# Performance work log

Measured on AMD Instinct MI355X. Metric: run time of the kernel, lower is better.

Reference implementation:

```python
import jax, jax.numpy as jnp
import numpy as np

B, S, H, V, NSPK = 8, 128, 768, 30000, 8


def gru_cell(x, h, wih, whh, bih, bhh):
    # torch GRU gate order: r, z, n
    gi = x @ wih.T + bih
    gh = h @ whh.T + bhh
    i_r, i_z, i_n = jnp.split(gi, 3, axis=-1)
    h_r, h_z, h_n = jnp.split(gh, 3, axis=-1)
    r = jax.nn.sigmoid(i_r + h_r)
    z = jax.nn.sigmoid(i_z + h_z)
    n = jnp.tanh(i_n + r * h_n)
    return (1.0 - z) * n + z * h


def setup_inputs() -> dict:
    key = jax.random.key(0)
    ks = jax.random.split(key, 32)
    nrm = lambda k, shp: (jax.random.normal(k, shp, dtype=jnp.float32) * 0.02)
    inp = {
        "chat_ids": jnp.arange(B, dtype=jnp.int32),
        "speaker_info": jax.random.randint(ks[0], (B, S), 0, NSPK),
        "sp_dialogues": jax.random.randint(ks[1], (B,), 0, NSPK),
        "sp_ind": jax.random.randint(ks[2], (B,), 0, NSPK),
        "inputs": jax.random.randint(ks[3], (B, S), 0, V),
        "emb": nrm(ks[4], (V, H)),
        # rnnD: GRU(E=H -> H)
        "d_wih": nrm(ks[5], (3 * H, H)), "d_whh": nrm(ks[6], (3 * H, H)),
        "d_bih": nrm(ks[7], (3 * H,)), "d_bhh": nrm(ks[8], (3 * H,)),
        # rnnG: GRU(3E -> H)
        "g_wih": nrm(ks[9], (3 * H, 3 * H)), "g_whh": nrm(ks[10], (3 * H, H)),
        "g_bih": nrm(ks[11], (3 * H,)), "g_bhh": nrm(ks[12], (3 * H,)),
        # rnnS: GRU(2E -> 2E)
        "s_wih": nrm(ks[13], (6 * H, 2 * H)), "s_whh": nrm(ks[14], (6 * H, 2 * H)),
        "s_bih": nrm(ks[15], (6 * H,)), "s_bhh": nrm(ks[16], (6 * H,)),
        # attention projections (qembed = kembed = hidden = E)
        "wq": nrm(ks[17], (H, H)), "bq": nrm(ks[18], (H,)),
        "wk": nrm(ks[19], (H, H)), "bk": nrm(ks[20], (H,)),
        "wv": nrm(ks[21], (H, H)), "bv": nrm(ks[22], (H,)),
        # fixed random initial states (torch.randn in forward)
        "h0": jax.random.normal(ks[23], (2 * H,), dtype=jnp.float32),
        "d_h0": jax.random.normal(ks[24], (H,), dtype=jnp.float32),
        "attn_h": jax.random.normal(ks[25], (H,), dtype=jnp.float32),
    }
    return inp


def _forward(chat_ids, speaker_info, inputs, emb,
             d_wih, d_whh, d_bih, d_bhh,
             g_wih, g_whh, g_bih, g_bhh,
             s_wih, s_whh, s_bih, s_bhh,
             wq, bq, wk, bk, wv, bv, h0, d_h0, attn_h):
    bert = emb[inputs]                              # [B,S,E]

    # rnnD over the whole dialogue (dropout is identity in eval)
    def d_step(h, x):
        h2 = gru_cell(x, h, d_wih, d_whh, d_bih, d_bhh)
        return h2, h2
    _, dlg = jax.lax.scan(d_step, jnp.zeros((B, H), bert.dtype), jnp.swapaxes(bert, 0, 1))
    dialogue = jnp.swapaxes(dlg, 0, 1)              # [B,S,H]

    speaker_seq = speaker_info[chat_ids]            # [B,S]
    scale = jnp.asarray(np.sqrt(H), dtype=dialogue.dtype)
    steps = jnp.arange(S)

    def batch_step(d_h, b_in):
        dlg_b, spk_b = b_in                         # [S,H], [S]
        op_buf0 = jnp.zeros((S, H), dialogue.dtype)
        sp0 = jnp.tile(h0[None, :], (NSPK, 1))      # every speaker starts at h0

        def step(carry, xs):
            op_buf, sp_states, dh = carry
            utt, spk, s = xs
            # growing-context attention over previously written op rows
            # (row s is still zero at this point, matching fop[b][:s+1])
            q = utt @ wq.T + bq                      # [H]
            K = op_buf @ wk.T + bk                   # [S,H]
            Vv = op_buf @ wv.T + bv                  # [S,H]
            scores = (K @ q) / scale                 # [S]
            mask = steps <= s
            probs = jax.nn.softmax(jnp.where(mask, scores, -jnp.inf))
            probs = jnp.where(jnp.isnan(probs), 0.0, probs)
            attn_out = probs @ Vv                    # [H]
            attn_part = jnp.where(s == 0, attn_h, attn_out)
            tmp = jnp.concatenate([attn_part, utt])  # [2H]
            h_spk = sp_states[spk]                   # dynamic speaker state
            h_new = gru_cell(tmp, h_spk, s_wih, s_whh, s_bih, s_bhh)
            spop_s = h_new + tmp                     # spop[b][s] = out + tmp
            sp_states = sp_states.at[spk].set(h_new)
            fop2_s = jnp.concatenate([spop_s, utt])  # [3H]
            op_s = gru_cell(fop2_s, dh, g_wih, g_whh, g_bih, g_bhh)
            op_buf = op_buf.at[s].set(op_s)
            return (op_buf, sp_states, op_s), (op_s, spop_s)

        (_, _, dh_out), (op_b, spop_b) = jax.lax.scan(
            step, (op_buf0, sp0, d_h), (dlg_b, spk_b, steps))
        return dh_out, (op_b, spop_b)

    # d_h carries across batch items, exactly as in the torch loop
    _, (op, spop) = jax.lax.scan(batch_step, d_h0, (dialogue, speaker_seq))
    return op, spop                                  # [B,S,H], [B,S,2H]


def reference(chat_ids, speaker_info, sp_dialogues, sp_ind, inputs, emb,
              d_wih, d_whh, d_bih, d_bhh,
              g_wih, g_whh, g_bih, g_bhh,
              s_wih, s_whh, s_bih, s_bhh,
              wq, bq, wk, bk, wv, bv, h0, d_h0, attn_h):
    return _forward(chat_ids, speaker_info, inputs, emb,
                    d_wih, d_whh, d_bih, d_bhh,
                    g_wih, g_whh, g_bih, g_bhh,
                    s_wih, s_whh, s_bih, s_bhh,
                    wq, bq, wk, bk, wv, bv, h0, d_h0, attn_h)
```

## Files before the change

### kernel.cpp

```cpp
#include <hip/hip_runtime.h>
#include <hip/hip_bf16.h>

typedef unsigned int uint32;
typedef unsigned short u16;
typedef unsigned long long u64;
typedef __attribute__((ext_vector_type(8))) short s16x8;
typedef __attribute__((ext_vector_type(4))) float f32x4;

#define H    768
#define H2   1536
#define H3   2304
#define H6   4608
#define BB   8
#define SS   128
#define GG   1024
#define NWG  256
#define NT   256
#define NTM  512
#define INVSCALE 0.036084391824351615f
#define SPIN_LIMIT (1 << 17)
#define DYN_LDS 163200

struct IN {
  const int *chat_ids, *speaker_info, *inputs;
  const float *emb, *d_wih, *d_whh, *d_bih, *d_bhh;
  const float *g_wih, *g_whh, *g_bih, *g_bhh;
  const float *s_wih, *s_whh, *s_bih, *s_bhh;
  const float *wq, *bq, *wk, *bk, *wv, *bv;
  const float *h0, *d_h0, *attn_h;
};

struct WS {
  int *flags1;
  float *Mqk, *Gsum;
  float *cu, *vkq, *cb, *cvs, *ch0s, *cvg, *chg0, *ghs0;
  float *Ms, *Mg;
  float *gi_d, *GIS;
  uint32 *gi_bf, *U_bf;
  float *dialogue, *U, *cvec, *GIG;
  float *gh_dbuf;
  float *sp_global;
  float *op_buf;
  u64 *op_tag;
  u64 *h_tag;
  u64 *sc_tag;
  float *probs_buf;
  float *h_buf, *Wbuf, *AO;
  float *out_op, *out_spop;
};

__device__ inline float sigm(float x) { return 1.f / (1.f + expf(-x)); }

__device__ inline u16 f2bf(float v) {
  __hip_bfloat16 b = __float2bfloat16(v);
  return *reinterpret_cast<u16*>(&b);
}
__device__ inline uint32 pack2bf(float a, float b) {
  return (uint32)f2bf(a) | ((uint32)f2bf(b) << 16);
}

__device__ inline float2 ld2(const float* p) { return *(const float2*)p; }
__device__ inline float2 ald2(const float* p) {
  u64 v = __hip_atomic_load((const u64*)p, __ATOMIC_RELAXED, __HIP_MEMORY_SCOPE_AGENT);
  union { u64 u; float2 f; } c; c.u = v; return c.f;
}
__device__ inline float ald(const float* p) {
  return __hip_atomic_load(p, __ATOMIC_RELAXED, __HIP_MEMORY_SCOPE_AGENT);
}
__device__ inline void ast(float* p, float v) {
  __hip_atomic_store(p, v, __ATOMIC_RELAXED, __HIP_MEMORY_SCOPE_AGENT);
}
__device__ inline void ast64(u64* p, u64 v) {
  __hip_atomic_store(p, v, __ATOMIC_RELAXED, __HIP_MEMORY_SCOPE_AGENT);
}
__device__ inline u64 ald64(const u64* p) {
  return __hip_atomic_load(p, __ATOMIC_RELAXED, __HIP_MEMORY_SCOPE_AGENT);
}
__device__ inline u64 tagf(int ep, float v) {
  return ((u64)(uint32)ep << 32) | (u64)__float_as_uint(v);
}

__device__ inline float pollf(const u64* p, int ep, int& bail) {
  int spins = 0;
  u64 v;
  for (;;) {
    v = ald64(p);
    if ((int)(v >> 32) >= ep) break;
    if (++spins > SPIN_LIMIT) { bail = 1; break; }
  }
  return __uint_as_float((uint32)v);
}

__device__ inline void gbar2(int* flags, int epoch, int& dead) {
  int bail = 0;
  __syncthreads();
  if (!dead) {
    if (threadIdx.x == 0)
      __hip_atomic_store(&flags[blockIdx.x * 16], epoch, __ATOMIC_RELAXED, __HIP_MEMORY_SCOPE_AGENT);
    if (threadIdx.x < NWG) {
      int spins = 0;
      while (__hip_atomic_load(&flags[threadIdx.x * 16], __ATOMIC_RELAXED, __HIP_MEMORY_SCOPE_AGENT) < epoch) {
        if (++spins > SPIN_LIMIT) { bail = 1; break; }
      }
    }
  }
  dead |= __syncthreads_or(bail);
  asm volatile("" ::: "memory");
}

template <int NI>
__device__ inline float dotr(const u16* wcol, const float2* xr) {
  const uint32* wp = (const uint32*)wcol;
  int l = threadIdx.x & 63;
  float acc = 0.f;
  #pragma unroll
  for (int i = 0; i < NI; i++) {
    uint32 u = wp[i * 64 + l];
    acc = fmaf(xr[i].x, __uint_as_float(u << 16),
          fmaf(xr[i].y, __uint_as_float(u & 0xffff0000u), acc));
  }
  #pragma unroll
  for (int o = 32; o > 0; o >>= 1) acc += __shfl_down(acc, o);
  return acc;
}
__device__ inline float xreduce(float a) {
  #pragma unroll
  for (int o = 32; o > 0; o >>= 1) a += __shfl_xor(a, o);
  return a;
}
template <int NI>
__device__ inline void loadx_lds(float2* xr, const float* x) {
  int l = threadIdx.x & 63;
  #pragma unroll
  for (int i = 0; i < NI; i++) xr[i] = ld2(x + 2 * (i * 64 + l));
}
template <int NI>
__device__ inline void loadx_atm(float2* xr, const float* x) {
  int l = threadIdx.x & 63;
  #pragma unroll
  for (int i = 0; i < NI; i++) xr[i] = ald2(x + 2 * (i * 64 + l));
}


__global__ __launch_bounds__(NT) void prep1_k(IN in, WS w) {
  long i = (long)blockIdx.x * NT + threadIdx.x;
  const long NG = (long)H3 * H;
  if (i < NG) {
    long n = i / H, k = i - n * H;
    w.Gsum[i] = in.g_wih[n * H3 + H + k] + in.g_wih[n * H3 + 2 * H + k];
  } else if (i < NG + H) {
    int m = (int)(i - NG);
    float a = 0.f;
    for (int t = 0; t < H; t++) a = fmaf(in.bq[t], in.wk[(long)t * H + m], a);
    w.cu[m] = a;
  } else if (i < NG + 2 * H) {
    int m = (int)(i - NG - H);
    float a = 0.f;
    for (int t = 0; t < H; t++) a = fmaf(in.bk[t], in.wq[(long)t * H + m], a);
    w.vkq[m] = a;
  } else if (i == NG + 2 * H) {
    float a = 0.f;
    for (int t = 0; t < H; t++) a = fmaf(in.bk[t], in.bq[t], a);
    w.cb[0] = a;
  }
}

__global__ __launch_bounds__(NT) void prep2_k(IN in, WS w) {
  int wid = blockIdx.x * (NT / 64) + (threadIdx.x >> 6);
  int l = threadIdx.x & 63;
  const int R1 = H6, R2 = H6 + H3, R3 = H6 + H3 + H6;
  if (wid < R1) {
    const float* row = in.s_wih + (long)wid * H2;
    float a = 0.f, c = 0.f;
    for (int i = l; i < H; i += 64) { float rv = row[i]; a = fmaf(in.bv[i], rv, a); c = fmaf(in.attn_h[i], rv, c); }
    #pragma unroll
    for (int o = 32; o > 0; o >>= 1) { a += __shfl_down(a, o); c += __shfl_down(c, o); }
    if (l == 0) { w.cvs[wid] = a; w.ch0s[wid] = c; }
  } else if (wid < R2) {
    int k = wid - R1;
    const float* row = in.g_wih + (long)k * H3;
    float a = 0.f, c = 0.f;
    for (int i = l; i < H; i += 64) { float rv = row[i]; a = fmaf(in.bv[i], rv, a); c = fmaf(in.attn_h[i], rv, c); }
    #pragma unroll
    for (int o = 32; o > 0; o >>= 1) { a += __shfl_down(a, o); c += __shfl_down(c, o); }
    if (l == 0) { w.cvg[k] = a; w.chg0[k] = c; }
  } else if (wid < R3) {
    int k = wid - R2;
    const float* row = in.s_whh + (long)k * H2;
    float a = 0.f;
    for (int i = l; i < H2; i += 64) a = fmaf(in.h0[i], row[i], a);
    #pragma unroll
    for (int o = 32; o > 0; o >>= 1) a += __shfl_down(a, o);
    if (l == 0) w.ghs0[k] = a + in.s_bhh[k];
  }
}

__global__ __launch_bounds__(NT) void pack_k(const float* src, uint32* dst, long n2) {
  long i = (long)blockIdx.x * NT + threadIdx.x;
  if (i < n2) dst[i] = pack2bf(src[2 * i], src[2 * i + 1]);
}

__global__ __launch_bounds__(NT) void gemm_k(const float* A, long sAm, long sAk,
                                             const float* B, long sBk,
                                             float* C, int M, int N, int K) {
  __shared__ float As[16][65];
  __shared__ float Bs[16][65];
  int m0 = blockIdx.y * 64, n0 = blockIdx.x * 64;
  int tid = threadIdx.x;
  int tx = tid & 15, ty = tid >> 4;
  float acc[4][4] = {};
  for (int k0 = 0; k0 < K; k0 += 16) {
    {
      int m = tid & 63, kb = tid >> 6;
      for (int p = 0; p < 4; p++) {
        int k = kb + p * 4;
        As[k][m] = A[(long)(m0 + m) * sAm + (long)(k0 + k) * sAk];
      }
    }
    {
      int n = tid & 63, kb = tid >> 6;
      for (int p = 0; p < 4; p++) {
        int k = kb + p * 4;
        Bs[k][n] = B[(long)(k0 + k) * sBk + (n0 + n)];
      }
    }
    __syncthreads();
    #pragma unroll
    for (int k = 0; k < 16; k++) {
      float a[4], b[4];
      #pragma unroll
      for (int i = 0; i < 4; i++) a[i] = As[k][ty * 4 + i];
      #pragma unroll
      for (int j = 0; j < 4; j++) b[j] = Bs[k][tx * 4 + j];
      #pragma unroll
      for (int i = 0; i < 4; i++)
        #pragma unroll
        for (int j = 0; j < 4; j++) acc[i][j] = fmaf(a[i], b[j], acc[i][j]);
    }
    __syncthreads();
  }
  for (int i = 0; i < 4; i++)
    for (int j = 0; j < 4; j++) {
      int m = m0 + ty * 4 + i, n = n0 + tx * 4 + j;
      C[(long)m * N + n] = acc[i][j];
    }
}

__global__ __launch_bounds__(NT) void mgemm_k(const float* A, long sAm, const int* gather,
                                              const float* B, long sB, int bColMajor,
                                              const float* bias, float* C, int N, int K) {
  __shared__ u16 Al[128 * 40];
  __shared__ u16 Bl[128 * 40];
  int tid = threadIdx.x;
  int n0 = blockIdx.x * 128, m0 = blockIdx.y * 128;
  int l = tid & 63, wv = tid >> 6;
  int wr = wv >> 1, wc = wv & 1;
  f32x4 acc[4][4] = {};
  long arow = gather ? (long)gather[m0 + (tid >> 1)] : (long)(m0 + (tid >> 1));
  for (int k0 = 0; k0 < K; k0 += 32) {
    __syncthreads();
    {
      int r = tid >> 1, half = tid & 1;
      const float* src = A + arow * sAm + k0 + half * 16;
      uint32* dst = (uint32*)(Al + r * 40 + half * 16);
      #pragma unroll
      for (int j = 0; j < 8; j++) dst[j] = pack2bf(src[2 * j], src[2 * j + 1]);
    }
    if (bColMajor) {
      int n = tid >> 1, half = tid & 1;
      const float* src = B + (long)(n0 + n) * sB + k0 + half * 16;
      uint32* dst = (uint32*)(Bl + n * 40 + half * 16);
      #pragma unroll
      for (int j = 0; j < 8; j++) dst[j] = pack2bf(src[2 * j], src[2 * j + 1]);
    } else {
      int kk = tid & 31, nb = tid >> 5;
      const float* src = B + (long)(k0 + kk) * sB + n0 + nb * 16;
      #pragma unroll
      for (int j = 0; j < 16; j++) Bl[(nb * 16 + j) * 40 + kk] = f2bf(src[j]);
    }
    __syncthreads();
    s16x8 af[4], bf[4];
    #pragma unroll
    for (int i = 0; i < 4; i++) {
      af[i] = *(const s16x8*)(Al + (wr * 64 + i * 16 + (l & 15)) * 40 + (l >> 4) * 8);
      bf[i] = *(const s16x8*)(Bl + (wc * 64 + i * 16 + (l & 15)) * 40 + (l >> 4) * 8);
    }
    #pragma unroll
    for (int i = 0; i < 4; i++)
      #pragma unroll
      for (int j = 0; j < 4; j++)
        acc[i][j] = __builtin_amdgcn_mfma_f32_16x16x32_bf16(af[i], bf[j], acc[i][j], 0, 0, 0);
  }
  #pragma unroll
  for (int i = 0; i < 4; i++)
    #pragma unroll
    for (int j = 0; j < 4; j++) {
      int n = n0 + wc * 64 + j * 16 + (l & 15);
      int mb = m0 + wr * 64 + i * 16 + ((l >> 4) << 2);
      float bb = bias ? bias[n] : 0.f;
      #pragma unroll
      for (int r = 0; r < 4; r++)
        C[(long)(mb + r) * N + n] = acc[i][j][r] + bb;
    }
}


__global__ __launch_bounds__(NTM) void coop_rnnD(IN in, WS w) {
  __shared__ u16 wD[9 * H];
  __shared__ float hB[BB][H];
  int tid = threadIdx.x, wg = blockIdx.x;
  int c0 = wg * 9;
  int l = tid & 63, wv = tid >> 6;
  for (int i = tid; i < 9 * H; i += NTM)
    wD[i] = f2bf(in.d_whh[(long)(c0 + i / H) * H + (i % H)]);
  __syncthreads();
  int epoch = 1, dead = 0;
  for (int t = 0; t < SS; t++) {
    if (t > 0) {
      float* ghb = w.gh_dbuf + (size_t)(t & 1) * BB * H3;
      for (int tk = wv; tk < 72; tk += 8) {
        int b = tk / 9, j = tk - b * 9;
        float2 xr[6];
        loadx_lds<6>(xr, hB[b]);
        float val = dotr<6>(wD + j * H, xr);
        if (l == 0) ast(ghb + (long)b * H3 + c0 + j, val + in.d_bhh[c0 + j]);
      }
      gbar2(w.flags1, epoch++, dead);
    }
    const float* ghb = w.gh_dbuf + (size_t)(t & 1) * BB * H3;
    for (int pc = tid; pc < BB * H / 2; pc += NTM) {
      int b = pc / (H / 2), k = 2 * (pc - b * (H / 2));
      const uint32* gi = w.gi_bf + ((long)(b * SS + t)) * (H3 / 2);
      uint32 u0 = gi[k >> 1], u1 = gi[(H + k) >> 1], u2 = gi[(2 * H + k) >> 1];
      float gr0 = __uint_as_float(u0 << 16), gr1 = __uint_as_float(u0 & 0xffff0000u);
      float gz0 = __uint_as_float(u1 << 16), gz1 = __uint_as_float(u1 & 0xffff0000u);
      float gn0 = __uint_as_float(u2 << 16), gn1 = __uint_as_float(u2 & 0xffff0000u);
      float hr0, hr1, hz0, hz1, hn0, hn1;
      if (t == 0) {
        hr0 = in.d_bhh[k]; hr1 = in.d_bhh[k + 1];
        hz0 = in.d_bhh[H + k]; hz1 = in.d_bhh[H + k + 1];
        hn0 = in.d_bhh[2 * H + k]; hn1 = in.d_bhh[2 * H + k + 1];
      } else {
        const float* gb = ghb + (long)b * H3;
        float2 a0 = ald2(gb + k), a1 = ald2(gb + H + k), a2 = ald2(gb + 2 * H + k);
        hr0 = a0.x; hr1 = a0.y; hz0 = a1.x; hz1 = a1.y; hn0 = a2.x; hn1 = a2.y;
      }
      float p0 = (t == 0) ? 0.f : hB[b][k], p1 = (t == 0) ? 0.f : hB[b][k + 1];
      float r0 = sigm(gr0 + hr0), r1 = sigm(gr1 + hr1);
      float z0 = sigm(gz0 + hz0), z1 = sigm(gz1 + hz1);
      float n0 = tanhf(gn0 + r0 * hn0), n1 = tanhf(gn1 + r1 * hn1);
      float h0v = (1.f - z0) * n0 + z0 * p0, h1v = (1.f - z1) * n1 + z1 * p1;
      hB[b][k] = h0v; hB[b][k + 1] = h1v;
      if (wg == 0) *(float2*)(w.dialogue + ((long)(b * SS + t)) * H + k) = make_float2(h0v, h1v);
    }
    __syncthreads();
  }
}

__global__ __launch_bounds__(NTM) void coop_main(IN in, WS w) {
  extern __shared__ char Lds[];
  u16*   wShh  = (u16*)(Lds + 0);
  u16*   wGab  = (u16*)(Lds + 55296);
  u16*   wMs   = (u16*)(Lds + 82944);
  u16*   wMg   = (u16*)(Lds + 110592);
  u16*   wGhh  = (u16*)(Lds + 124416);
  float* OPMSl = (float*)(Lds + 138240);
  float* OPMGl = (float*)(Lds + 147968);
  float* h_lds = (float*)(Lds + 152576);
  float* op_lds= (float*)(Lds + 158720);
  float* el    = (float*)(Lds + 161792);
  float* red   = (float*)(Lds + 162304);
  float* loc_si  = (float*)(Lds + 162560);
  float* loc_ghs = (float*)(Lds + 162632);
  float* loc_gw  = (float*)(Lds + 162776);
  float* loc_ghg = (float*)(Lds + 162812);
  float* loc_gih = (float*)(Lds + 162848);
  float* loc_gis = (float*)(Lds + 162884);
  float* loc_gig = (float*)(Lds + 162956);
  float* spc     = (float*)(Lds + 162992);

  int tid = threadIdx.x, wg = blockIdx.x;
  int l = tid & 63, wv = tid >> 6;
  int c0s = wg * 6, c0g3 = wg * 3;
  auto rrS = [&](int j) { return (j / 6) * H2 + c0s + (j % 6); };
  auto rrG = [&](int j) { return (j / 3) * H + c0g3 + (j % 3); };

  for (int i = tid; i < 18 * H2; i += NTM) { int j = i / H2, k = i - j * H2; wShh[i] = f2bf(in.s_whh[(long)rrS(j) * H2 + k]); }
  for (int i = tid; i < 9 * H2;  i += NTM) { int j = i / H2, k = i - j * H2; wGab[i] = f2bf(in.g_wih[(long)rrG(j) * H3 + k]); }
  for (int i = tid; i < 18 * H;  i += NTM) { int j = i / H,  k = i - j * H;  wMs[i]  = f2bf(w.Ms[(long)rrS(j) * H + k]); }
  for (int i = tid; i < 9 * H;   i += NTM) { int j = i / H,  k = i - j * H;  wMg[i]  = f2bf(w.Mg[(long)rrG(j) * H + k]); }
  for (int i = tid; i < 9 * H;   i += NTM) { int j = i / H,  k = i - j * H;  wGhh[i] = f2bf(in.g_whh[(long)rrG(j) * H + k]); }
  for (int i = tid; i < H; i += NTM) op_lds[i] = in.d_h0[i];
  __syncthreads();

  int dead = 0;

  for (int g = 0; g < GG; g++) {
    int s = g & 127, b = g >> 7;
    int g1 = g + 1, s1 = g1 & 127;
    int spk_cur = in.speaker_info[in.chat_ids[b] * SS + s];
    int spk_next = (g1 < GG) ? in.speaker_info[in.chat_ids[g1 >> 7] * SS + s1] : 0;
    float cv = w.cvec[g];
    if (tid < 18) loc_gis[tid] = w.GIS[(long)g * H6 + rrS(tid)];

    int bail = 0;
    if (!dead) {
      if (g > 0 && tid < 384) {
        int c = tid * 2;
        float v0 = pollf(w.op_tag + c, g, bail);
        float v1 = pollf(w.op_tag + c + 1, g, bail);
        op_lds[c] = v0; op_lds[c + 1] = v1;
      } else if (tid >= 384 && s >= 1) {
        int j = tid - 384;
        if (j <= s - 2)
          el[j] = expf(fminf(pollf(w.sc_tag + (size_t)(g & 1) * SS + j, g, bail), 30.f));
      }
    }
    dead |= __syncthreads_or(bail);

    if (s >= 1) {
      float2 xr[6];
      loadx_lds<6>(xr, op_lds);
      float a = 0.f;
      {
        const uint32* Ub = w.U_bf + (long)g * (H / 2);
        #pragma unroll
        for (int i = 0; i < 6; i++) {
          uint32 u = Ub[i * 64 + l];
          int idx = 2 * (i * 64 + l);
          a = fmaf(op_lds[idx], __uint_as_float(u << 16),
              fmaf(op_lds[idx + 1], __uint_as_float(u & 0xffff0000u), a));
        }
        a = xreduce(a);
      }
      float e1 = expf(fminf(a + cv, 30.f));
      float bs = 0.f;
      if (l <= s - 2) bs = el[l];
      if (l + 64 <= s - 2) bs += el[l + 64];
      bs = xreduce(bs);
      float suinv = 1.f / (e1 + bs + expf(fminf(cv, 30.f)));

      for (int r = wv; r < 36; r += 8) {
        if (r < 18) {
          float nr = dotr<6>(wMs + r * H, xr);
          float aa = 0.f;
          if (l <= s - 2) aa = el[l] * OPMSl[l * 19 + r];
          if (l + 64 <= s - 2) aa = fmaf(el[l + 64], OPMSl[(l + 64) * 19 + r], aa);
          #pragma unroll
          for (int o = 32; o > 0; o >>= 1) aa += __shfl_down(aa, o);
          if (l == 0) {
            OPMSl[(s - 1) * 19 + r] = nr;
            loc_si[r] = (aa + e1 * nr) * suinv + w.cvs[rrS(r)];
          }
        } else if (r < 27) {
          int t = r - 18;
          float nr = dotr<6>(wMg + t * H, xr);
          float aa = 0.f;
          if (l <= s - 2) aa = el[l] * OPMGl[l * 9 + t];
          if (l + 64 <= s - 2) aa = fmaf(el[l + 64], OPMGl[(l + 64) * 9 + t], aa);
          #pragma unroll
          for (int o = 32; o > 0; o >>= 1) aa += __shfl_down(aa, o);
          if (l == 0) {
            OPMGl[(s - 1) * 9 + t] = nr;
            loc_gw[t] = (aa + e1 * nr) * suinv + w.cvg[rrG(t)];
          }
        } else {
          int t = r - 27;
          float v = dotr<6>(wGhh + t * H, xr);
          if (l == 0) loc_ghg[t] = v + in.g_bhh[rrG(t)];
        }
      }
      if (g1 < GG && s1 != 0 && spk_next != spk_cur) {
        float2 xs[12];
        loadx_atm<12>(xs, w.sp_global + (long)spk_next * H2);
        for (int t = wv; t < 18; t += 8) {
          float v = dotr<12>(wShh + t * H2, xs);
          if (l == 0) loc_ghs[(g1 & 1) * 18 + t] = v + in.s_bhh[rrS(t)];
        }
      }
      if (wv == 7 && g1 < GG && s1 >= 2 && wg < s) {
        const float* opr = w.op_buf + (long)wg * H;
        const uint32* Ub1 = w.U_bf + (long)g1 * (H / 2);
        float a2 = 0.f;
        #pragma unroll
        for (int i0 = 0; i0 < 6; i0++) {
          int idx = i0 * 64 + l;
          float2 xa = ald2(opr + 2 * idx);
          uint32 u = Ub1[idx];
          a2 = fmaf(xa.x, __uint_as_float(u << 16),
               fmaf(xa.y, __uint_as_float(u & 0xffff0000u), a2));
        }
        #pragma unroll
        for (int o = 32; o > 0; o >>= 1) a2 += __shfl_down(a2, o);
        if (l == 0) ast64(w.sc_tag + (size_t)(g1 & 1) * SS + wg, tagf(g1, a2 + w.cvec[g1]));
      }
      if (wg == 0 && wv == 6) {
        int j = l;
        float pv = (j <= s - 2) ? el[j] * suinv : ((j == s - 1) ? e1 * suinv : 0.f);
        w.probs_buf[(long)g * SS + j] = pv;
        j = l + 64;
        pv = (j <= s - 2) ? el[j] * suinv : ((j == s - 1) ? e1 * suinv : 0.f);
        w.probs_buf[(long)g * SS + j] = pv;
      }
      __syncthreads();
    } else {
      if (tid < 18) loc_si[tid] = w.ch0s[rrS(tid)];
      else if (tid >= 32 && tid < 41) loc_gw[tid - 32] = w.chg0[rrG(tid - 32)];
      if (tid >= 64 && tid < 112) { int x = (tid - 64) / 6, t2 = (tid - 64) % 6; spc[x * 6 + t2] = in.h0[c0s + t2]; }
      if (tid >= 128 && tid < 176) {
        int x = (tid - 128) / 6, t2 = (tid - 128) % 6;
        if (x != spk_cur) ast(w.sp_global + (long)x * H2 + c0s + t2, in.h0[c0s + t2]);
      }
      if (wv == 3) {
        float2 xr[6];
        loadx_lds<6>(xr, op_lds);
        for (int j = 0; j < 9; j++) {
          float val = dotr<6>(wGhh + j * H, xr);
          if (l == 0) loc_ghg[j] = val + in.g_bhh[rrG(j)];
        }
      }
      if (wg == 0 && tid >= 384) w.probs_buf[(long)g * SS + (tid - 384)] = 0.f;
      __syncthreads();
    }

    float op_prev = (tid < 3) ? op_lds[c0g3 + tid] : 0.f;

    if (tid < 6) {
      int c = c0s + tid;
      float hprev = spc[spk_cur * 6 + tid];
      float ghr, ghz, ghn;
      if (s == 0) { ghr = w.ghs0[c]; ghz = w.ghs0[H2 + c]; ghn = w.ghs0[2 * H2 + c]; }
      else { const float* gb = loc_ghs + (g & 1) * 18; ghr = gb[tid]; ghz = gb[6 + tid]; ghn = gb[12 + tid]; }
      float gir = loc_gis[tid] + loc_si[tid];
      float giz = loc_gis[6 + tid] + loc_si[6 + tid];
      float gin = loc_gis[12 + tid] + loc_si[12 + tid];
      float r = sigm(gir + ghr), z = sigm(giz + ghz);
      float n = tanhf(gin + r * ghn);
      float hn = (1.f - z) * n + z * hprev;
      spc[spk_cur * 6 + tid] = hn;
      ast64(w.h_tag + c, tagf(g1, hn));
      ast(w.sp_global + (long)spk_cur * H2 + c, hn);
      w.h_buf[(long)g * H2 + c] = hn;
    }

    if (tid < 9) loc_gig[tid] = w.GIG[(long)g * H3 + rrG(tid)];
    bail = 0;
    if (!dead) {
      int c = tid * 3;
      float v0 = pollf(w.h_tag + c, g1, bail);
      float v1 = pollf(w.h_tag + c + 1, g1, bail);
      float v2 = pollf(w.h_tag + c + 2, g1, bail);
      h_lds[c] = v0; h_lds[c + 1] = v1; h_lds[c + 2] = v2;
    }
    dead |= __syncthreads_or(bail);

    {
      int needsh = (g1 < GG && s1 != 0 && (spk_next == spk_cur || s == 0)) ? 1 : 0;
      int diff = (spk_next != spk_cur);
      if (needsh) {
        float2 xs[12];
        if (diff) loadx_atm<12>(xs, w.sp_global + (long)spk_next * H2);
        else loadx_lds<12>(xs, h_lds);
        for (int t = wv; t < 18; t += 8) {
          float val = dotr<12>(wShh + t * H2, xs);
          if (l == 0) loc_ghs[(g1 & 1) * 18 + t] = val + in.s_bhh[rrS(t)];
        }
      }
      {
        float2 xh[12];
        loadx_lds<12>(xh, h_lds);
        for (int t = wv; t < 9; t += 8) {
          float val = dotr<12>(wGab + t * H2, xh);
          if (l == 0) loc_gih[t] = val;
        }
      }
    }
    __syncthreads();

    if (tid < 3) {
      int c = c0g3 + tid;
      float gir = loc_gig[tid]     + loc_gw[tid]     + loc_gih[tid];
      float giz = loc_gig[3 + tid] + loc_gw[3 + tid] + loc_gih[3 + tid];
      float gin = loc_gig[6 + tid] + loc_gw[6 + tid] + loc_gih[6 + tid];
      float r = sigm(gir + loc_ghg[tid]);
      float z = sigm(giz + loc_ghg[3 + tid]);
      float n = tanhf(gin + r * loc_ghg[6 + tid]);
      float o = (1.f - z) * n + z * op_prev;
      ast64(w.op_tag + c, tagf(g1, o));
      ast(w.op_buf + (long)s * H + c, o);
      w.out_op[(long)g * H + c] = o;
    }
  }
}


__global__ __launch_bounds__(NT) void fixup_u_k(WS w) {
  long i = (long)blockIdx.x * NT + threadIdx.x;
  if (i < (long)GG * H) {
    int m = (int)(i % H);
    w.U[i] = (w.U[i] + w.cu[m]) * INVSCALE;
  }
}

__global__ __launch_bounds__(NT) void cvec_k(WS w) {
  int g = blockIdx.x * 4 + (threadIdx.x >> 6);
  int l = threadIdx.x & 63;
  const float* d = w.dialogue + (long)g * H;
  float p = 0.f;
  for (int i = l; i < H; i += 64) p = fmaf(d[i], w.vkq[i], p);
  #pragma unroll
  for (int o = 32; o > 0; o >>= 1) p += __shfl_down(p, o);
  if (l == 0) w.cvec[g] = (p + w.cb[0]) * INVSCALE;
}

__global__ __launch_bounds__(NT) void epi_W_k(WS w) {
  int g = blockIdx.x, b = g >> 7;
  __shared__ float pl[SS];
  if (threadIdx.x < SS) pl[threadIdx.x] = w.probs_buf[(long)g * SS + threadIdx.x];
  __syncthreads();
  const float* opb = w.out_op + (long)b * SS * H;
  for (int n = threadIdx.x; n < H; n += NT) {
    float acc = 0.f;
    for (int j = 0; j < SS; j++) acc = fmaf(pl[j], opb[(long)j * H + n], acc);
    w.Wbuf[(long)g * H + n] = acc;
  }
}

__global__ __launch_bounds__(NT) void assemble_k(IN in, WS w) {
  long idx = (long)blockIdx.x * NT + threadIdx.x;
  if (idx >= (long)GG * H2) return;
  long g = idx / H2;
  int k = (int)(idx - g * H2);
  int s = (int)(g & 127);
  float t;
  if (k < H) t = (s == 0) ? in.attn_h[k] : w.AO[g * H + k];
  else t = w.dialogue[g * H + (k - H)];
  w.out_spop[idx] = w.h_buf[idx] + t;
}


extern "C" void kernel_launch(void* const* d_in, const int* in_sizes, int n_in,
                              void* d_out, int out_size, void* d_ws, size_t ws_size,
                              hipStream_t stream) {
  IN in;
  in.chat_ids = (const int*)d_in[0];
  in.speaker_info = (const int*)d_in[1];
  in.inputs = (const int*)d_in[4];
  in.emb = (const float*)d_in[5];
  in.d_wih = (const float*)d_in[6];  in.d_whh = (const float*)d_in[7];
  in.d_bih = (const float*)d_in[8];  in.d_bhh = (const float*)d_in[9];
  in.g_wih = (const float*)d_in[10]; in.g_whh = (const float*)d_in[11];
  in.g_bih = (const float*)d_in[12]; in.g_bhh = (const float*)d_in[13];
  in.s_wih = (const float*)d_in[14]; in.s_whh = (const float*)d_in[15];
  in.s_bih = (const float*)d_in[16]; in.s_bhh = (const float*)d_in[17];
  in.wq = (const float*)d_in[18];  in.bq = (const float*)d_in[19];
  in.wk = (const float*)d_in[20];  in.bk = (const float*)d_in[21];
  in.wv = (const float*)d_in[22];  in.bv = (const float*)d_in[23];
  in.h0 = (const float*)d_in[24];  in.d_h0 = (const float*)d_in[25];
  in.attn_h = (const float*)d_in[26];

  char* base = (char*)d_ws;
  size_t off = 0;
  auto A = [&](size_t bytes) -> void* {
    size_t r = (off + 255) & ~(size_t)255;
    off = r + bytes;
    return (void*)(base + r);
  };
  WS w;
  w.flags1 = (int*)A(NWG * 16 * 4);
  w.Mqk = (float*)A((size_t)H * H * 4);
  w.Gsum = (float*)A((size_t)H3 * H * 4);
  w.cu = (float*)A(H * 4);
  w.vkq = (float*)A(H * 4);
  w.cb = (float*)A(4);
  w.cvs = (float*)A(H6 * 4);
  w.ch0s = (float*)A(H6 * 4);
  w.cvg = (float*)A(H3 * 4);
  w.chg0 = (float*)A(H3 * 4);
  w.ghs0 = (float*)A(H6 * 4);
  w.Ms = (float*)A((size_t)H6 * H * 4);
  w.Mg = (float*)A((size_t)H3 * H * 4);
  {
    void* r1 = A((size_t)GG * H6 * 4);
    w.gi_d = (float*)r1;
    w.GIS = (float*)r1;
  }
  w.gi_bf = (uint32*)A((size_t)GG * H3 * 2);
  w.U_bf = (uint32*)A((size_t)GG * H * 2);
  w.dialogue = (float*)A((size_t)GG * H * 4);
  w.U = (float*)A((size_t)GG * H * 4);
  w.cvec = (float*)A(GG * 4);
  w.GIG = (float*)A((size_t)GG * H3 * 4);
  w.gh_dbuf = (float*)A((size_t)2 * BB * H3 * 4);
  w.sp_global = (float*)A((size_t)BB * H2 * 4);
  w.op_buf = (float*)A((size_t)SS * H * 4);
  w.op_tag = (u64*)A((size_t)H * 8);
  w.h_tag = (u64*)A((size_t)H2 * 8);
  w.sc_tag = (u64*)A((size_t)2 * SS * 8);
  w.probs_buf = (float*)A((size_t)GG * SS * 4);
  w.h_buf = (float*)A((size_t)GG * H2 * 4);
  w.Wbuf = (float*)A((size_t)GG * H * 4);
  w.AO = (float*)A((size_t)GG * H * 4);
  w.out_op = (float*)d_out;
  w.out_spop = (float*)d_out + (size_t)GG * H;

  (void)hipFuncSetAttribute((const void*)coop_main, hipFuncAttributeMaxDynamicSharedMemorySize, DYN_LDS);

  (void)hipMemsetAsync(w.flags1, 0, NWG * 16 * 4, stream);
  (void)hipMemsetAsync(w.op_tag, 0, (size_t)H * 8, stream);
  (void)hipMemsetAsync(w.h_tag, 0, (size_t)H2 * 8, stream);
  (void)hipMemsetAsync(w.sc_tag, 0, (size_t)2 * SS * 8, stream);

  const long NG = (long)H3 * H;
  prep1_k<<<(int)((NG + 2 * H + 1 + NT - 1) / NT), NT, 0, stream>>>(in, w);
  prep2_k<<<(H6 + H3 + H6 + 3) / 4, NT, 0, stream>>>(in, w);

  gemm_k<<<dim3(H / 64, H / 64), NT, 0, stream>>>(in.wq, 1, H, in.wk, H, w.Mqk, H, H, H);
  mgemm_k<<<dim3(H / 128, H6 / 128), NT, 0, stream>>>(in.s_wih, H2, nullptr, in.wv, H, 0, nullptr, w.Ms, H, H);
  mgemm_k<<<dim3(H / 128, H3 / 128), NT, 0, stream>>>(in.g_wih, H3, nullptr, in.wv, H, 0, nullptr, w.Mg, H, H);
  mgemm_k<<<dim3(H3 / 128, GG / 128), NT, 0, stream>>>(in.emb, H, in.inputs, in.d_wih, H, 1, in.d_bih, w.gi_d, H3, H);
  pack_k<<<(int)(((long)GG * H3 / 2 + NT - 1) / NT), NT, 0, stream>>>(w.gi_d, w.gi_bf, (long)GG * H3 / 2);
  coop_rnnD<<<NWG, NTM, 0, stream>>>(in, w);

  mgemm_k<<<dim3(H / 128, GG / 128), NT, 0, stream>>>(w.dialogue, H, nullptr, w.Mqk, H, 0, nullptr, w.U, H, H);
  mgemm_k<<<dim3(H6 / 128, GG / 128), NT, 0, stream>>>(w.dialogue, H, nullptr, in.s_wih + H, H2, 1, in.s_bih, w.GIS, H6, H);
  mgemm_k<<<dim3(H3 / 128, GG / 128), NT, 0, stream>>>(w.dialogue, H, nullptr, w.Gsum, H, 1, in.g_bih, w.GIG, H3, H);
  fixup_u_k<<<(GG * H + NT - 1) / NT, NT, 0, stream>>>(w);
  pack_k<<<(int)(((long)GG * H / 2 + NT - 1) / NT), NT, 0, stream>>>(w.U, w.U_bf, (long)GG * H / 2);
  cvec_k<<<GG / 4, NT, 0, stream>>>(w);

  coop_main<<<NWG, NTM, DYN_LDS, stream>>>(in, w);

  epi_W_k<<<GG, NT, 0, stream>>>(w);
  mgemm_k<<<dim3(H / 128, GG / 128), NT, 0, stream>>>(w.Wbuf, H, nullptr, in.wv, H, 1, in.bv, w.AO, H, H);
  assemble_k<<<(int)(((long)GG * H2 + NT - 1) / NT), NT, 0, stream>>>(in, w);
}
```

Measured before the change: 13.78 ms.

## Fuse speaker GRU update into per-wave attention work and drop a barrier

Reassigns work across the 8 waves. Waves 0-5 each compute three speaker-GRU input rows (r, z, n for one column), apply the GRU update directly in registers and publish the new hidden value. Waves 6 and 7 handle the global-GRU attention rows, the probability output, the recurrent g_hh projection and the next-step score prefetch. This removes the __syncthreads and the separate tid<6 gate stage that sat on the critical path between steps. In exchange the per-wave load is less even, and the published h now depends on loc_ghs and loc_gis having been written before this point without a barrier.

After: 14.32 ms. 4.0% more time.

```diff
diff --git a/kernel.cpp b/kernel.cpp
--- a/kernel.cpp
+++ b/kernel.cpp
@@ -418,9 +418,12 @@
     }
     dead |= __syncthreads_or(bail);
 
+    float op_prev = (tid < 3) ? op_lds[c0g3 + tid] : 0.f;
+
+    float2 xr[6];
+    loadx_lds<6>(xr, op_lds);
+
     if (s >= 1) {
-      float2 xr[6];
-      loadx_lds<6>(xr, op_lds);
       float a = 0.f;
       {
         const uint32* Ub = w.U_bf + (long)g * (H / 2);
@@ -440,20 +443,45 @@
       bs = xreduce(bs);
       float suinv = 1.f / (e1 + bs + expf(fminf(cv, 30.f)));
 
-      for (int r = wv; r < 36; r += 8) {
-        if (r < 18) {
+      if (wv < 6) {
+        float si[3];
+        #pragma unroll
+        for (int k = 0; k < 3; k++) {
+          int r = wv + 6 * k;
           float nr = dotr<6>(wMs + r * H, xr);
           float aa = 0.f;
           if (l <= s - 2) aa = el[l] * OPMSl[l * 19 + r];
           if (l + 64 <= s - 2) aa = fmaf(el[l + 64], OPMSl[(l + 64) * 19 + r], aa);
           #pragma unroll
           for (int o = 32; o > 0; o >>= 1) aa += __shfl_down(aa, o);
-          if (l == 0) {
-            OPMSl[(s - 1) * 19 + r] = nr;
-            loc_si[r] = (aa + e1 * nr) * suinv + w.cvs[rrS(r)];
+          if (l == 0) OPMSl[(s - 1) * 19 + r] = nr;
+          si[k] = (aa + e1 * nr) * suinv + w.cvs[rrS(r)];
+        }
+        if (l == 0) {
+          int c = c0s + wv;
+          float hprev = spc[spk_cur * 6 + wv];
+          const float* gb = loc_ghs + (g & 1) * 18;
+          float r_ = sigm(loc_gis[wv] + si[0] + gb[wv]);
+          float z_ = sigm(loc_gis[6 + wv] + si[1] + gb[6 + wv]);
+          float n_ = tanhf(loc_gis[12 + wv] + si[2] + r_ * gb[12 + wv]);
+          float hn = (1.f - z_) * n_ + z_ * hprev;
+          spc[spk_cur * 6 + wv] = hn;
+          ast64(w.h_tag + c, tagf(g1, hn));
+          ast(w.sp_global + (long)spk_cur * H2 + c, hn);
+          w.h_buf[(long)g * H2 + c] = hn;
+        }
+        if (g1 < GG && s1 != 0 && spk_next != spk_cur) {
+          float2 xs[12];
+          loadx_atm<12>(xs, w.sp_global + (long)spk_next * H2);
+          #pragma unroll
+          for (int k = 0; k < 3; k++) {
+            int r = wv + 6 * k;
+            float v = dotr<12>(wShh + r * H2, xs);
+            if (l == 0) loc_ghs[(g1 & 1) * 18 + r] = v + in.s_bhh[rrS(r)];
           }
-        } else if (r < 27) {
-          int t = r - 18;
+        }
+      } else if (wv == 6) {
+        for (int t = 0; t < 9; t++) {
           float nr = dotr<6>(wMg + t * H, xr);
           float aa = 0.f;
           if (l <= s - 2) aa = el[l] * OPMGl[l * 9 + t];
@@ -464,83 +492,69 @@
             OPMGl[(s - 1) * 9 + t] = nr;
             loc_gw[t] = (aa + e1 * nr) * suinv + w.cvg[rrG(t)];
           }
-        } else {
-          int t = r - 27;
+        }
+        if (wg == 0) {
+          int j = l;
+          float pv = (j <= s - 2) ? el[j] * suinv : ((j == s - 1) ? e1 * suinv : 0.f);
+          w.probs_buf[(long)g * SS + j] = pv;
+          j = l + 64;
+          pv = (j <= s - 2) ? el[j] * suinv : ((j == s - 1) ? e1 * suinv : 0.f);
+          w.probs_buf[(long)g * SS + j] = pv;
+        }
+      } else {
+        for (int t = 0; t < 9; t++) {
           float v = dotr<6>(wGhh + t * H, xr);
           if (l == 0) loc_ghg[t] = v + in.g_bhh[rrG(t)];
         }
-      }
-      if (g1 < GG && s1 != 0 && spk_next != spk_cur) {
-        float2 xs[12];
-        loadx_atm<12>(xs, w.sp_global + (long)spk_next * H2);
-        for (int t = wv; t < 18; t += 8) {
-          float v = dotr<12>(wShh + t * H2, xs);
-          if (l == 0) loc_ghs[(g1 & 1) * 18 + t] = v + in.s_bhh[rrS(t)];
-        }
-      }
-      if (wv == 7 && g1 < GG && s1 >= 2 && wg < s) {
-        const float* opr = w.op_buf + (long)wg * H;
-        const uint32* Ub1 = w.U_bf + (long)g1 * (H / 2);
-        float a2 = 0.f;
-        #pragma unroll
-        for (int i0 = 0; i0 < 6; i0++) {
-          int idx = i0 * 64 + l;
-          float2 xa = ald2(opr + 2 * idx);
-          uint32 u = Ub1[idx];
-          a2 = fmaf(xa.x, __uint_as_float(u << 16),
-               fmaf(xa.y, __uint_as_float(u & 0xffff0000u), a2));
-        }
-        #pragma unroll
-        for (int o = 32; o > 0; o >>= 1) a2 += __shfl_down(a2, o);
-        if (l == 0) ast64(w.sc_tag + (size_t)(g1 & 1) * SS + wg, tagf(g1, a2 + w.cvec[g1]));
-      }
-      if (wg == 0 && wv == 6) {
-        int j = l;
-        float pv = (j <= s - 2) ? el[j] * suinv : ((j == s - 1) ? e1 * suinv : 0.f);
-        w.probs_buf[(long)g * SS + j] = pv;
-        j = l + 64;
-        pv = (j <= s - 2) ? el[j] * suinv : ((j == s - 1) ? e1 * suinv : 0.f);
-        w.probs_buf[(long)g * SS + j] = pv;
-      }
-      __syncthreads();
+        if (g1 < GG && s1 >= 2 && wg < s) {
+          const float* opr = w.op_buf + (long)wg * H;
+          const uint32* Ub1 = w.U_bf + (long)g1 * (H / 2);
+          float a2 = 0.f;
+          #pragma unroll
+          for (int i0 = 0; i0 < 6; i0++) {
+            int idx = i0 * 64 + l;
+            float2 xa = ald2(opr + 2 * idx);
+            uint32 u = Ub1[idx];
+            a2 = fmaf(xa.x, __uint_as_float(u << 16),
+                 fmaf(xa.y, __uint_as_float(u & 0xffff0000u), a2));
+          }
+          #pragma unroll
+          for (int o = 32; o > 0; o >>= 1) a2 += __shfl_down(a2, o);
+          if (l == 0) ast64(w.sc_tag + (size_t)(g1 & 1) * SS + wg, tagf(g1, a2 + w.cvec[g1]));
+        }
+      }
     } else {
-      if (tid < 18) loc_si[tid] = w.ch0s[rrS(tid)];
-      else if (tid >= 32 && tid < 41) loc_gw[tid - 32] = w.chg0[rrG(tid - 32)];
-      if (tid >= 64 && tid < 112) { int x = (tid - 64) / 6, t2 = (tid - 64) % 6; spc[x * 6 + t2] = in.h0[c0s + t2]; }
-      if (tid >= 128 && tid < 176) {
-        int x = (tid - 128) / 6, t2 = (tid - 128) % 6;
-        if (x != spk_cur) ast(w.sp_global + (long)x * H2 + c0s + t2, in.h0[c0s + t2]);
-      }
-      if (wv == 3) {
-        float2 xr[6];
-        loadx_lds<6>(xr, op_lds);
-        for (int j = 0; j < 9; j++) {
-          float val = dotr<6>(wGhh + j * H, xr);
-          if (l == 0) loc_ghg[j] = val + in.g_bhh[rrG(j)];
-        }
-      }
-      if (wg == 0 && tid >= 384) w.probs_buf[(long)g * SS + (tid - 384)] = 0.f;
-      __syncthreads();
-    }
-
-    float op_prev = (tid < 3) ? op_lds[c0g3 + tid] : 0.f;
-
-    if (tid < 6) {
-      int c = c0s + tid;
-      float hprev = spc[spk_cur * 6 + tid];
-      float ghr, ghz, ghn;
-      if (s == 0) { ghr = w.ghs0[c]; ghz = w.ghs0[H2 + c]; ghn = w.ghs0[2 * H2 + c]; }
-      else { const float* gb = loc_ghs + (g & 1) * 18; ghr = gb[tid]; ghz = gb[6 + tid]; ghn = gb[12 + tid]; }
-      float gir = loc_gis[tid] + loc_si[tid];
-      float giz = loc_gis[6 + tid] + loc_si[6 + tid];
-      float gin = loc_gis[12 + tid] + loc_si[12 + tid];
-      float r = sigm(gir + ghr), z = sigm(giz + ghz);
-      float n = tanhf(gin + r * ghn);
-      float hn = (1.f - z) * n + z * hprev;
-      spc[spk_cur * 6 + tid] = hn;
-      ast64(w.h_tag + c, tagf(g1, hn));
-      ast(w.sp_global + (long)spk_cur * H2 + c, hn);
-      w.h_buf[(long)g * H2 + c] = hn;
+      if (wv < 6) {
+        if (l == 0) {
+          int c = c0s + wv;
+          float h0v = in.h0[c];
+          #pragma unroll
+          for (int x = 0; x < 8; x++) spc[x * 6 + wv] = h0v;
+          float r_ = sigm(loc_gis[wv] + w.ch0s[rrS(wv)] + w.ghs0[c]);
+          float z_ = sigm(loc_gis[6 + wv] + w.ch0s[rrS(6 + wv)] + w.ghs0[H2 + c]);
+          float n_ = tanhf(loc_gis[12 + wv] + w.ch0s[rrS(12 + wv)] + r_ * w.ghs0[2 * H2 + c]);
+          float hn = (1.f - z_) * n_ + z_ * h0v;
+          spc[spk_cur * 6 + wv] = hn;
+          ast64(w.h_tag + c, tagf(g1, hn));
+          ast(w.sp_global + (long)spk_cur * H2 + c, hn);
+          w.h_buf[(long)g * H2 + c] = hn;
+        }
+        if (l >= 1 && l <= 8) {
+          int x = l - 1;
+          if (x != spk_cur) ast(w.sp_global + (long)x * H2 + c0s + wv, in.h0[c0s + wv]);
+        }
+      } else if (wv == 6) {
+        if (l < 9) loc_gw[l] = w.chg0[rrG(l)];
+        if (wg == 0) {
+          w.probs_buf[(long)g * SS + l] = 0.f;
+          w.probs_buf[(long)g * SS + l + 64] = 0.f;
+        }
+      } else {
+        for (int t = 0; t < 9; t++) {
+          float v = dotr<6>(wGhh + t * H, xr);
+          if (l == 0) loc_ghg[t] = v + in.g_bhh[rrG(t)];
+        }
+      }
     }
 
     if (tid < 9) loc_gig[tid] = w.GIG[(long)g * H3 + rrG(tid)];
```
